# Kernel tuning notes

Measured on AMD Instinct MI355X. Metric: run time of the kernel, lower is better.

## Reference

```python
import jax, jax.numpy as jnp
import numpy as np

MAPP = jnp.array([0.5, 1.0, 1.5, 2.0], dtype=jnp.float32)  # magnitude constellation (len = one_hot_len)


def setup_inputs() -> dict:
    key = jax.random.key(0)
    ks = jax.random.split(key, 20)
    B, BL, SM = 512, 256, 8
    S = BL + SM            # sym_len = 264
    V, Z, OH = 128, 1024, 4
    inp = {}
    inp["l"] = 0
    inp["x_mag"] = jax.random.uniform(ks[0], (1, B, S), jnp.float32)
    inp["x_mag_oh"] = jax.random.normal(ks[1], (B, S * OH), jnp.float32)
    inp["v"] = jax.random.normal(ks[2], (B, V), jnp.float32)
    inp["x_phase"] = jax.random.normal(ks[3], (1, B, S), jnp.float32)
    inp["y_e"] = jax.random.normal(ks[4], (B, BL), jnp.float32)
    inp["y_o"] = jax.random.normal(ks[5], (B, BL), jnp.float32)
    inp["Psi_e"] = jax.random.normal(ks[6], (B, 2 * BL, 2 * S), jnp.float32) * 0.1
    inp["Psi_o"] = jax.random.normal(ks[7], (B, 2 * BL, 2 * S), jnp.float32) * 0.1
    # Linear params, std=0.01 as in torch init
    inp["W1"] = jax.random.normal(ks[8], (Z, S + V), jnp.float32) * 0.01
    inp["b1"] = jax.random.normal(ks[9], (Z,), jnp.float32) * 0.01
    inp["W2"] = jax.random.normal(ks[10], (S * OH, Z), jnp.float32) * 0.01
    inp["b2"] = jax.random.normal(ks[11], (S * OH,), jnp.float32) * 0.01
    inp["W3"] = jax.random.normal(ks[12], (V, Z), jnp.float32) * 0.01
    inp["b3"] = jax.random.normal(ks[13], (V,), jnp.float32) * 0.01
    inp["d1"] = jax.random.uniform(ks[14], (1,), jnp.float32)
    inp["d2"] = jax.random.uniform(ks[15], (1,), jnp.float32)
    inp["d3"] = jax.random.uniform(ks[16], (1,), jnp.float32)
    inp["d4"] = jax.random.uniform(ks[17], (1,), jnp.float32)
    return inp


def reference(l, x_mag, x_mag_oh, v, x_phase, y_e, y_o, Psi_e, Psi_o,
              W1, b1, W2, b2, W3, b3, d1, d2, d3, d4):
    B, S = x_phase.shape[1], x_phase.shape[2]
    BL = y_e.shape[1]
    mag, ph = x_mag[-1], x_phase[-1]          # [B,S]
    c, s = jnp.cos(ph), jnp.sin(ph)
    x = jnp.concatenate([mag * c, mag * s], axis=-1)  # [B,2S]

    def A_and_sql(Psi):
        # Psi: [B, 2*BL, 2*S]
        Px = jnp.einsum('bms,bs->bm', Psi, x)         # [B, 2*BL]
        a, b_ = Px[:, :BL], Px[:, BL:]
        # Psi^T @ blockdiag(a,b) == row-scale Psi (avoids diag_embed+bmm):
        # M[b,j,i] = Psi[b,j,i]*a[b,j] + Psi[b,BL+j,i]*b[b,j]  -> [B, BL, 2S]
        M = Psi[:, :BL, :] * a[:, :, None] + Psi[:, BL:, :] * b_[:, :, None]
        # jacobian @ (Psi^T D) == cos/sin row-scaling of the two S-halves:
        A = (c[:, :, None] * jnp.swapaxes(M[:, :, :S], 1, 2)
             + s[:, :, None] * jnp.swapaxes(M[:, :, S:], 1, 2))  # [B, S, BL]
        sql = a * a + b_ * b_                          # [B, BL]
        return A, sql

    A_e, sql_e = A_and_sql(Psi_e)
    A_o, sql_o = A_and_sql(Psi_o)
    mv = lambda A, y: jnp.einsum('bsk,bk->bs', A, y)
    # NOTE: original code uses delta2 for the A_o@y_o term (delta3 unused) -- kept faithful.
    q = (mag - d1 * mv(A_e, y_e) + d2 * mv(A_e, sql_e)
         - d2 * mv(A_o, y_o) + d4 * mv(A_o, sql_o))    # [B,S]

    z = jax.nn.relu(jnp.concatenate([q, v], axis=1) @ W1.T + b1)   # [B,Z]
    x_mag_oh_new = x_mag_oh + z @ W2.T + b2                        # [B,S*OH]
    # oh_2_sym: softmax over one-hot dim, expectation over constellation
    sym = jax.nn.softmax(x_mag_oh_new.reshape(B, S, -1), axis=-1) @ MAPP  # [B,S]
    x_mag_new = jnp.concatenate([x_mag, sym[None]], axis=0)
    v_new = v + z @ W3.T + b3
    return (x_mag_new, x_mag_oh_new, v_new)
```

## Files before the change

kernel.cpp:

```cpp
#include <hip/hip_runtime.h>

#define S_     264
#define BL_    256
#define TWO_S  528
#define TWO_BL 512
#define B_     512
#define V_     128
#define NQ     392
#define Z_     1024
#define N2_    1056
#define NTOT   1184

__global__ __launch_bounds__(256, 4) void k_psi(
    const float* __restrict__ x_mag, const float* __restrict__ x_phase,
    const float* __restrict__ y_e, const float* __restrict__ y_o,
    const float* __restrict__ Psi_e, const float* __restrict__ Psi_o,
    const float* __restrict__ d1, const float* __restrict__ d2,
    const float* __restrict__ d4,
    float* __restrict__ contrib)
{
    const int tid = threadIdx.x;
    const int b   = blockIdx.x >> 1;
    const int psi = blockIdx.x & 1;
    const float* Psi = psi ? Psi_o : Psi_e;
    const float* yv  = psi ? y_o  : y_e;
    const float coefY = psi ? -d2[0] : -d1[0];
    const float coefS = psi ?  d4[0] :  d2[0];

    __shared__ float4 xs4s[132];
    __shared__ float  cs[S_], sn[S_];
    __shared__ float  ys[BL_];
    __shared__ float4 redTy4[4][132];
    __shared__ float4 redTs4[4][132];

    float* xs = (float*)xs4s;

    for (int s = tid; s < S_; s += 256) {
        float mag = x_mag[(size_t)b * S_ + s];
        float ph  = x_phase[(size_t)b * S_ + s];
        float c = cosf(ph), si = sinf(ph);
        cs[s] = c; sn[s] = si;
        xs[s]      = mag * c;
        xs[S_ + s] = mag * si;
    }
    ys[tid] = yv[(size_t)b * BL_ + tid];
    __syncthreads();

    const int wave = tid >> 6, lane = tid & 63;
    const float4 f4z = {0.f, 0.f, 0.f, 0.f};

    float4 x0 = xs4s[lane];
    float4 x1 = xs4s[lane + 64];
    float4 x2 = (lane < 4) ? xs4s[lane + 128] : f4z;

    float4 ty0 = f4z, ty1 = f4z, ty2 = f4z;
    float4 ts0 = f4z, ts1 = f4z, ts2 = f4z;

    const float4* Pg = (const float4*)(Psi + (size_t)b * TWO_BL * TWO_S);

    int pair = wave;
    float4 l0, l1, l2 = f4z, h0, h1, h2 = f4z;
    {
        const float4* rl = Pg + (size_t)pair * 132;
        const float4* rh = rl + (size_t)BL_ * 132;
        l0 = rl[lane]; l1 = rl[lane + 64];
        h0 = rh[lane]; h1 = rh[lane + 64];
        if (lane < 4) { l2 = rl[lane + 128]; h2 = rh[lane + 128]; }
    }

    while (pair < BL_) {
        const int nxt = pair + 4;
        float4 nl0 = f4z, nl1 = f4z, nl2 = f4z;
        float4 nh0 = f4z, nh1 = f4z, nh2 = f4z;
        if (nxt < BL_) {
            const float4* rl = Pg + (size_t)nxt * 132;
            const float4* rh = rl + (size_t)BL_ * 132;
            nl0 = rl[lane]; nl1 = rl[lane + 64];
            nh0 = rh[lane]; nh1 = rh[lane + 64];
            if (lane < 4) { nl2 = rl[lane + 128]; nh2 = rh[lane + 128]; }
        }

        float a  = l0.x*x0.x + l0.y*x0.y + l0.z*x0.z + l0.w*x0.w
                 + l1.x*x1.x + l1.y*x1.y + l1.z*x1.z + l1.w*x1.w
                 + l2.x*x2.x + l2.y*x2.y + l2.z*x2.z + l2.w*x2.w;
        float bb = h0.x*x0.x + h0.y*x0.y + h0.z*x0.z + h0.w*x0.w
                 + h1.x*x1.x + h1.y*x1.y + h1.z*x1.z + h1.w*x1.w
                 + h2.x*x2.x + h2.y*x2.y + h2.z*x2.z + h2.w*x2.w;
        #pragma unroll
        for (int off = 32; off; off >>= 1) {
            a  += __shfl_xor(a, off);
            bb += __shfl_xor(bb, off);
        }

        const float yy  = ys[pair];
        const float sq  = a * a + bb * bb;
        const float cyl = a * yy, cyh = bb * yy;
        const float csl = a * sq, csh = bb * sq;

        ty0.x += l0.x*cyl + h0.x*cyh; ty0.y += l0.y*cyl + h0.y*cyh;
        ty0.z += l0.z*cyl + h0.z*cyh; ty0.w += l0.w*cyl + h0.w*cyh;
        ty1.x += l1.x*cyl + h1.x*cyh; ty1.y += l1.y*cyl + h1.y*cyh;
        ty1.z += l1.z*cyl + h1.z*cyh; ty1.w += l1.w*cyl + h1.w*cyh;
        ty2.x += l2.x*cyl + h2.x*cyh; ty2.y += l2.y*cyl + h2.y*cyh;
        ty2.z += l2.z*cyl + h2.z*cyh; ty2.w += l2.w*cyl + h2.w*cyh;

        ts0.x += l0.x*csl + h0.x*csh; ts0.y += l0.y*csl + h0.y*csh;
        ts0.z += l0.z*csl + h0.z*csh; ts0.w += l0.w*csl + h0.w*csh;
        ts1.x += l1.x*csl + h1.x*csh; ts1.y += l1.y*csl + h1.y*csh;
        ts1.z += l1.z*csl + h1.z*csh; ts1.w += l1.w*csl + h1.w*csh;
        ts2.x += l2.x*csl + h2.x*csh; ts2.y += l2.y*csl + h2.y*csh;
        ts2.z += l2.z*csl + h2.z*csh; ts2.w += l2.w*csl + h2.w*csh;

        pair = nxt;
        l0 = nl0; l1 = nl1; l2 = nl2;
        h0 = nh0; h1 = nh1; h2 = nh2;
    }

    redTy4[wave][lane]      = ty0;  redTy4[wave][lane + 64] = ty1;
    redTs4[wave][lane]      = ts0;  redTs4[wave][lane + 64] = ts1;
    if (lane < 4) {
        redTy4[wave][lane + 128] = ty2;
        redTs4[wave][lane + 128] = ts2;
    }
    __syncthreads();

    const float* redTy = (const float*)redTy4;
    const float* redTs = (const float*)redTs4;
    float* outp = contrib + (size_t)(b * 2 + psi) * S_;
    for (int s = tid; s < S_; s += 256) {
        float tyl = 0.f, tyh = 0.f, tsl = 0.f, tsh = 0.f;
        #pragma unroll
        for (int w = 0; w < 4; ++w) {
            tyl += redTy[w * TWO_S + s];
            tyh += redTy[w * TWO_S + S_ + s];
            tsl += redTs[w * TWO_S + s];
            tsh += redTs[w * TWO_S + S_ + s];
        }
        float mvy = cs[s] * tyl + sn[s] * tyh;
        float mvs = cs[s] * tsl + sn[s] * tsh;
        outp[s] = coefY * mvy + coefS * mvs;
    }
}

__global__ __launch_bounds__(256) void k_gemm1(
    const float* __restrict__ x_mag, const float* __restrict__ contrib,
    const float* __restrict__ v, const float* __restrict__ W1,
    const float* __restrict__ b1, float* __restrict__ z)
{
    const int tid = threadIdx.x;
    const int m0  = blockIdx.x * 32;
    const int n0  = blockIdx.y * 64;
    const int tr  = (tid >> 4) & 1 ? 0 : 0;
    const int trow = ((tid >> 4)) * 2;
    const int tcol = (tid & 15) * 4;

    __shared__ float As[16][36];
    __shared__ float Ws[16][68];

    float acc[2][4] = {};

    const int kr  = tid >> 2;
    const int kk4 = (tid & 3) * 4;

    for (int kc = 0; kc < NQ; kc += 16) {
        if (tid < 128) {
            const int arow = m0 + kr;
            const int gk = kc + kk4;
            float4 vv = {0.f, 0.f, 0.f, 0.f};
            if (gk < NQ) {
                if (gk + 3 < S_) {
                    float4 xm = *(const float4*)&x_mag[(size_t)arow * S_ + gk];
                    float4 ce = *(const float4*)&contrib[(size_t)(arow * 2) * S_ + gk];
                    float4 co = *(const float4*)&contrib[(size_t)(arow * 2 + 1) * S_ + gk];
                    vv.x = xm.x + ce.x + co.x; vv.y = xm.y + ce.y + co.y;
                    vv.z = xm.z + ce.z + co.z; vv.w = xm.w + ce.w + co.w;
                } else if (gk >= S_) {
                    vv = *(const float4*)&v[(size_t)arow * V_ + (gk - S_)];
                }
            }
            As[kk4 + 0][kr] = vv.x; As[kk4 + 1][kr] = vv.y;
            As[kk4 + 2][kr] = vv.z; As[kk4 + 3][kr] = vv.w;
        }
        {
            const int wrow = n0 + kr;
            const int gk = kc + kk4;
            float4 vv = {0.f, 0.f, 0.f, 0.f};
            if (gk + 3 < NQ) {
                vv = *(const float4*)&W1[(size_t)wrow * NQ + gk];
            } else if (gk < NQ) {
                const float* wp = W1 + (size_t)wrow * NQ + gk;
                vv.x = wp[0];
                if (gk + 1 < NQ) vv.y = wp[1];
                if (gk + 2 < NQ) vv.z = wp[2];
            }
            Ws[kk4 + 0][kr] = vv.x; Ws[kk4 + 1][kr] = vv.y;
            Ws[kk4 + 2][kr] = vv.z; Ws[kk4 + 3][kr] = vv.w;
        }
        __syncthreads();

        #pragma unroll
        for (int k = 0; k < 16; ++k) {
            float2 a2 = *(const float2*)&As[k][trow];
            float4 w4 = *(const float4*)&Ws[k][tcol];
            acc[0][0] += a2.x * w4.x; acc[0][1] += a2.x * w4.y;
            acc[0][2] += a2.x * w4.z; acc[0][3] += a2.x * w4.w;
            acc[1][0] += a2.y * w4.x; acc[1][1] += a2.y * w4.y;
            acc[1][2] += a2.y * w4.z; acc[1][3] += a2.y * w4.w;
        }
        __syncthreads();
    }

    #pragma unroll
    for (int i = 0; i < 2; ++i) {
        const int row = m0 + trow + i;
        const int col = n0 + tcol;
        float4 r;
        r.x = fmaxf(acc[i][0] + b1[col + 0], 0.f);
        r.y = fmaxf(acc[i][1] + b1[col + 1], 0.f);
        r.z = fmaxf(acc[i][2] + b1[col + 2], 0.f);
        r.w = fmaxf(acc[i][3] + b1[col + 3], 0.f);
        *(float4*)&z[(size_t)row * Z_ + col] = r;
    }
}

__global__ __launch_bounds__(256) void k_gemm23(
    const float* __restrict__ z,
    const float* __restrict__ W2, const float* __restrict__ b2,
    const float* __restrict__ oh,
    const float* __restrict__ W3, const float* __restrict__ b3,
    const float* __restrict__ v,
    float* __restrict__ out_oh, float* __restrict__ out_v)
{
    const int tid = threadIdx.x;
    const int m0  = blockIdx.x * 32;
    const int n0  = blockIdx.y * 64;
    const int trow = (tid >> 4) * 2;
    const int tcol = (tid & 15) * 4;

    __shared__ float As[16][36];
    __shared__ float Ws[16][68];

    float acc[2][4] = {};

    const int kr  = tid >> 2;
    const int kk4 = (tid & 3) * 4;

    for (int kc = 0; kc < Z_; kc += 16) {
        if (tid < 128) {
            const int arow = m0 + kr;
            float4 vv = *(const float4*)&z[(size_t)arow * Z_ + kc + kk4];
            As[kk4 + 0][kr] = vv.x; As[kk4 + 1][kr] = vv.y;
            As[kk4 + 2][kr] = vv.z; As[kk4 + 3][kr] = vv.w;
        }
        {
            const int wrow = n0 + kr;
            float4 vv = {0.f, 0.f, 0.f, 0.f};
            if (wrow < NTOT) {
                const float* wp = (wrow < N2_)
                    ? (W2 + (size_t)wrow * Z_)
                    : (W3 + (size_t)(wrow - N2_) * Z_);
                vv = *(const float4*)&wp[kc + kk4];
            }
            Ws[kk4 + 0][kr] = vv.x; Ws[kk4 + 1][kr] = vv.y;
            Ws[kk4 + 2][kr] = vv.z; Ws[kk4 + 3][kr] = vv.w;
        }
        __syncthreads();

        #pragma unroll
        for (int k = 0; k < 16; ++k) {
            float2 a2 = *(const float2*)&As[k][trow];
            float4 w4 = *(const float4*)&Ws[k][tcol];
            acc[0][0] += a2.x * w4.x; acc[0][1] += a2.x * w4.y;
            acc[0][2] += a2.x * w4.z; acc[0][3] += a2.x * w4.w;
            acc[1][0] += a2.y * w4.x; acc[1][1] += a2.y * w4.y;
            acc[1][2] += a2.y * w4.z; acc[1][3] += a2.y * w4.w;
        }
        __syncthreads();
    }

    #pragma unroll
    for (int i = 0; i < 2; ++i) {
        const int row = m0 + trow + i;
        const int col = n0 + tcol;
        if (col + 3 < N2_) {
            float4 ad = *(const float4*)&oh[(size_t)row * N2_ + col];
            float4 r;
            r.x = acc[i][0] + b2[col + 0] + ad.x;
            r.y = acc[i][1] + b2[col + 1] + ad.y;
            r.z = acc[i][2] + b2[col + 2] + ad.z;
            r.w = acc[i][3] + b2[col + 3] + ad.w;
            *(float4*)&out_oh[(size_t)row * N2_ + col] = r;
        } else if (col < NTOT) {
            const int c3 = col - N2_;
            float4 ad = *(const float4*)&v[(size_t)row * V_ + c3];
            float4 r;
            r.x = acc[i][0] + b3[c3 + 0] + ad.x;
            r.y = acc[i][1] + b3[c3 + 1] + ad.y;
            r.z = acc[i][2] + b3[c3 + 2] + ad.z;
            r.w = acc[i][3] + b3[c3 + 3] + ad.w;
            *(float4*)&out_v[(size_t)row * V_ + c3] = r;
        }
    }
}

__global__ void k_final(const float* __restrict__ x_mag,
                        const float* __restrict__ oh_new,
                        float* __restrict__ out0)
{
    int idx = blockIdx.x * 256 + threadIdx.x;
    if (idx >= B_ * S_) return;
    out0[idx] = x_mag[idx];
    const float* p = oh_new + (size_t)idx * 4;
    float a0 = p[0], a1 = p[1], a2 = p[2], a3 = p[3];
    float m  = fmaxf(fmaxf(a0, a1), fmaxf(a2, a3));
    float e0 = expf(a0 - m), e1 = expf(a1 - m), e2 = expf(a2 - m), e3 = expf(a3 - m);
    float sum = e0 + e1 + e2 + e3;
    float sym = (0.5f * e0 + 1.0f * e1 + 1.5f * e2 + 2.0f * e3) / sum;
    out0[B_ * S_ + idx] = sym;
}

extern "C" void kernel_launch(void* const* d_in, const int* in_sizes, int n_in,
                              void* d_out, int out_size, void* d_ws, size_t ws_size,
                              hipStream_t stream)
{
    const float* x_mag    = (const float*)d_in[1];
    const float* x_mag_oh = (const float*)d_in[2];
    const float* v        = (const float*)d_in[3];
    const float* x_phase  = (const float*)d_in[4];
    const float* y_e      = (const float*)d_in[5];
    const float* y_o      = (const float*)d_in[6];
    const float* Psi_e    = (const float*)d_in[7];
    const float* Psi_o    = (const float*)d_in[8];
    const float* W1       = (const float*)d_in[9];
    const float* b1       = (const float*)d_in[10];
    const float* W2       = (const float*)d_in[11];
    const float* b2       = (const float*)d_in[12];
    const float* W3       = (const float*)d_in[13];
    const float* b3       = (const float*)d_in[14];
    const float* d1       = (const float*)d_in[15];
    const float* d2       = (const float*)d_in[16];
    const float* d4       = (const float*)d_in[18];

    float* ws      = (float*)d_ws;
    float* contrib = ws;
    float* z       = contrib + 1024 * S_;

    float* out0   = (float*)d_out;
    float* out_oh = out0 + 2 * B_ * S_;
    float* out_v  = out_oh + B_ * N2_;

    k_psi<<<dim3(B_ * 2), dim3(256), 0, stream>>>(
        x_mag, x_phase, y_e, y_o, Psi_e, Psi_o, d1, d2, d4, contrib);

    k_gemm1<<<dim3(16, 16), dim3(256), 0, stream>>>(
        x_mag, contrib, v, W1, b1, z);

    k_gemm23<<<dim3(16, 19), dim3(256), 0, stream>>>(
        z, W2, b2, x_mag_oh, W3, b3, v, out_oh, out_v);

    k_final<<<dim3((B_ * S_ + 255) / 256), dim3(256), 0, stream>>>(
        x_mag, out_oh, out0);
}
```

Measured before the change: 314.1 us.

## Merge Psi accumulators, deepen prefetch, widen GEMM K tiles, fuse final softmax

The Psi kernel folds the y and squared-norm weights into a single scalar per row pair. That leaves one accumulator set instead of two, halving the FMA work and the shared reduction. It also double-buffers two row pairs ahead, so more global loads are in flight. Both GEMMs now stage 32-deep K tiles with all threads loading, which halves the barrier count. The separate final kernel is removed: the x_mag copy moves into the Psi kernel and the softmax expectation into the GEMM23 epilogue, saving a launch and a re-read of out_oh. The trade-off is higher register pressure in the Psi kernel and more shared memory in the GEMMs.

```diff
diff --git a/kernel.cpp b/kernel.cpp
--- a/kernel.cpp
+++ b/kernel.cpp
@@ -17,7 +17,7 @@
     const float* __restrict__ Psi_e, const float* __restrict__ Psi_o,
     const float* __restrict__ d1, const float* __restrict__ d2,
     const float* __restrict__ d4,
-    float* __restrict__ contrib)
+    float* __restrict__ contrib, float* __restrict__ out0)
 {
     const int tid = threadIdx.x;
     const int b   = blockIdx.x >> 1;
@@ -29,9 +29,8 @@
 
     __shared__ float4 xs4s[132];
     __shared__ float  cs[S_], sn[S_];
-    __shared__ float  ys[BL_];
-    __shared__ float4 redTy4[4][132];
-    __shared__ float4 redTs4[4][132];
+    __shared__ float  gys[BL_];
+    __shared__ float4 redU4[4][132];
 
     float* xs = (float*)xs4s;
 
@@ -42,8 +41,9 @@
         cs[s] = c; sn[s] = si;
         xs[s]      = mag * c;
         xs[S_ + s] = mag * si;
-    }
-    ys[tid] = yv[(size_t)b * BL_ + tid];
+        if (psi == 0) out0[(size_t)b * S_ + s] = mag;
+    }
+    gys[tid] = coefY * yv[(size_t)b * BL_ + tid];
     __syncthreads();
 
     const int wave = tid >> 6, lane = tid & 63;
@@ -53,92 +53,77 @@
     float4 x1 = xs4s[lane + 64];
     float4 x2 = (lane < 4) ? xs4s[lane + 128] : f4z;
 
-    float4 ty0 = f4z, ty1 = f4z, ty2 = f4z;
-    float4 ts0 = f4z, ts1 = f4z, ts2 = f4z;
+    float4 u0 = f4z, u1 = f4z, u2 = f4z;
 
     const float4* Pg = (const float4*)(Psi + (size_t)b * TWO_BL * TWO_S);
 
-    int pair = wave;
-    float4 l0, l1, l2 = f4z, h0, h1, h2 = f4z;
-    {
-        const float4* rl = Pg + (size_t)pair * 132;
-        const float4* rh = rl + (size_t)BL_ * 132;
-        l0 = rl[lane]; l1 = rl[lane + 64];
-        h0 = rh[lane]; h1 = rh[lane + 64];
-        if (lane < 4) { l2 = rl[lane + 128]; h2 = rh[lane + 128]; }
-    }
-
-    while (pair < BL_) {
-        const int nxt = pair + 4;
-        float4 nl0 = f4z, nl1 = f4z, nl2 = f4z;
-        float4 nh0 = f4z, nh1 = f4z, nh2 = f4z;
-        if (nxt < BL_) {
-            const float4* rl = Pg + (size_t)nxt * 132;
-            const float4* rh = rl + (size_t)BL_ * 132;
-            nl0 = rl[lane]; nl1 = rl[lane + 64];
-            nh0 = rh[lane]; nh1 = rh[lane + 64];
-            if (lane < 4) { nl2 = rl[lane + 128]; nh2 = rh[lane + 128]; }
-        }
-
-        float a  = l0.x*x0.x + l0.y*x0.y + l0.z*x0.z + l0.w*x0.w
-                 + l1.x*x1.x + l1.y*x1.y + l1.z*x1.z + l1.w*x1.w
-                 + l2.x*x2.x + l2.y*x2.y + l2.z*x2.z + l2.w*x2.w;
-        float bb = h0.x*x0.x + h0.y*x0.y + h0.z*x0.z + h0.w*x0.w
-                 + h1.x*x1.x + h1.y*x1.y + h1.z*x1.z + h1.w*x1.w
-                 + h2.x*x2.x + h2.y*x2.y + h2.z*x2.z + h2.w*x2.w;
-        #pragma unroll
-        for (int off = 32; off; off >>= 1) {
-            a  += __shfl_xor(a, off);
-            bb += __shfl_xor(bb, off);
-        }
-
-        const float yy  = ys[pair];
-        const float sq  = a * a + bb * bb;
-        const float cyl = a * yy, cyh = bb * yy;
-        const float csl = a * sq, csh = bb * sq;
-
-        ty0.x += l0.x*cyl + h0.x*cyh; ty0.y += l0.y*cyl + h0.y*cyh;
-        ty0.z += l0.z*cyl + h0.z*cyh; ty0.w += l0.w*cyl + h0.w*cyh;
-        ty1.x += l1.x*cyl + h1.x*cyh; ty1.y += l1.y*cyl + h1.y*cyh;
-        ty1.z += l1.z*cyl + h1.z*cyh; ty1.w += l1.w*cyl + h1.w*cyh;
-        ty2.x += l2.x*cyl + h2.x*cyh; ty2.y += l2.y*cyl + h2.y*cyh;
-        ty2.z += l2.z*cyl + h2.z*cyh; ty2.w += l2.w*cyl + h2.w*cyh;
-
-        ts0.x += l0.x*csl + h0.x*csh; ts0.y += l0.y*csl + h0.y*csh;
-        ts0.z += l0.z*csl + h0.z*csh; ts0.w += l0.w*csl + h0.w*csh;
-        ts1.x += l1.x*csl + h1.x*csh; ts1.y += l1.y*csl + h1.y*csh;
-        ts1.z += l1.z*csl + h1.z*csh; ts1.w += l1.w*csl + h1.w*csh;
-        ts2.x += l2.x*csl + h2.x*csh; ts2.y += l2.y*csl + h2.y*csh;
-        ts2.z += l2.z*csl + h2.z*csh; ts2.w += l2.w*csl + h2.w*csh;
-
-        pair = nxt;
-        l0 = nl0; l1 = nl1; l2 = nl2;
-        h0 = nh0; h1 = nh1; h2 = nh2;
-    }
-
-    redTy4[wave][lane]      = ty0;  redTy4[wave][lane + 64] = ty1;
-    redTs4[wave][lane]      = ts0;  redTs4[wave][lane + 64] = ts1;
-    if (lane < 4) {
-        redTy4[wave][lane + 128] = ty2;
-        redTs4[wave][lane + 128] = ts2;
-    }
+#define LOADF(PP, L0, L1, L2, H0, H1, H2) {                         \
+        const float4* rl_ = Pg + (size_t)(PP) * 132;                \
+        const float4* rh_ = rl_ + (size_t)BL_ * 132;                \
+        L0 = rl_[lane]; L1 = rl_[lane + 64];                        \
+        H0 = rh_[lane]; H1 = rh_[lane + 64];                        \
+        if (lane < 4) { L2 = rl_[lane + 128]; H2 = rh_[lane + 128]; } \
+        else          { L2 = f4z; H2 = f4z; }                       \
+    }
+
+#define COMPUTE(L0, L1, L2, H0, H1, H2, PIDX) {                     \
+        float a  = L0.x*x0.x + L0.y*x0.y + L0.z*x0.z + L0.w*x0.w    \
+                 + L1.x*x1.x + L1.y*x1.y + L1.z*x1.z + L1.w*x1.w    \
+                 + L2.x*x2.x + L2.y*x2.y + L2.z*x2.z + L2.w*x2.w;   \
+        float bb = H0.x*x0.x + H0.y*x0.y + H0.z*x0.z + H0.w*x0.w    \
+                 + H1.x*x1.x + H1.y*x1.y + H1.z*x1.z + H1.w*x1.w    \
+                 + H2.x*x2.x + H2.y*x2.y + H2.z*x2.z + H2.w*x2.w;   \
+        _Pragma("unroll")                                           \
+        for (int off_ = 32; off_; off_ >>= 1) {                     \
+            a  += __shfl_xor(a, off_);                              \
+            bb += __shfl_xor(bb, off_);                             \
+        }                                                           \
+        float g  = gys[PIDX] + coefS * (a * a + bb * bb);           \
+        float wl = a * g, wh = bb * g;                              \
+        u0.x += L0.x*wl + H0.x*wh;  u0.y += L0.y*wl + H0.y*wh;      \
+        u0.z += L0.z*wl + H0.z*wh;  u0.w += L0.w*wl + H0.w*wh;      \
+        u1.x += L1.x*wl + H1.x*wh;  u1.y += L1.y*wl + H1.y*wh;      \
+        u1.z += L1.z*wl + H1.z*wh;  u1.w += L1.w*wl + H1.w*wh;      \
+        u2.x += L2.x*wl + H2.x*wh;  u2.y += L2.y*wl + H2.y*wh;      \
+        u2.z += L2.z*wl + H2.z*wh;  u2.w += L2.w*wl + H2.w*wh;      \
+    }
+
+    float4 al0, al1, al2, ah0, ah1, ah2;
+    float4 bl0, bl1, bl2, bh0, bh1, bh2;
+    LOADF(wave,     al0, al1, al2, ah0, ah1, ah2);
+    LOADF(wave + 4, bl0, bl1, bl2, bh0, bh1, bh2);
+
+    for (int j = 0; j < 64; j += 2) {
+        const int pA = wave + 4 * j;
+        const int pC = (j + 2 < 64) ? pA + 8  : 0;
+        const int pD = (j + 3 < 64) ? pA + 12 : 0;
+        float4 cl0, cl1, cl2, ch0, ch1, ch2;
+        LOADF(pC, cl0, cl1, cl2, ch0, ch1, ch2);
+        COMPUTE(al0, al1, al2, ah0, ah1, ah2, pA);
+        float4 dl0, dl1, dl2, dh0, dh1, dh2;
+        LOADF(pD, dl0, dl1, dl2, dh0, dh1, dh2);
+        COMPUTE(bl0, bl1, bl2, bh0, bh1, bh2, pA + 4);
+        al0 = cl0; al1 = cl1; al2 = cl2; ah0 = ch0; ah1 = ch1; ah2 = ch2;
+        bl0 = dl0; bl1 = dl1; bl2 = dl2; bh0 = dh0; bh1 = dh1; bh2 = dh2;
+    }
+#undef LOADF
+#undef COMPUTE
+
+    redU4[wave][lane]      = u0;
+    redU4[wave][lane + 64] = u1;
+    if (lane < 4) redU4[wave][lane + 128] = u2;
     __syncthreads();
 
-    const float* redTy = (const float*)redTy4;
-    const float* redTs = (const float*)redTs4;
+    const float* redU = (const float*)redU4;
     float* outp = contrib + (size_t)(b * 2 + psi) * S_;
     for (int s = tid; s < S_; s += 256) {
-        float tyl = 0.f, tyh = 0.f, tsl = 0.f, tsh = 0.f;
+        float ul = 0.f, uh = 0.f;
         #pragma unroll
         for (int w = 0; w < 4; ++w) {
-            tyl += redTy[w * TWO_S + s];
-            tyh += redTy[w * TWO_S + S_ + s];
-            tsl += redTs[w * TWO_S + s];
-            tsh += redTs[w * TWO_S + S_ + s];
-        }
-        float mvy = cs[s] * tyl + sn[s] * tyh;
-        float mvs = cs[s] * tsl + sn[s] * tsh;
-        outp[s] = coefY * mvy + coefS * mvs;
+            ul += redU[w * TWO_S + s];
+            uh += redU[w * TWO_S + S_ + s];
+        }
+        outp[s] = cs[s] * ul + sn[s] * uh;
     }
 }
 
@@ -150,56 +135,48 @@
     const int tid = threadIdx.x;
     const int m0  = blockIdx.x * 32;
     const int n0  = blockIdx.y * 64;
-    const int tr  = (tid >> 4) & 1 ? 0 : 0;
-    const int trow = ((tid >> 4)) * 2;
+    const int trow = (tid >> 4) * 2;
     const int tcol = (tid & 15) * 4;
 
-    __shared__ float As[16][36];
-    __shared__ float Ws[16][68];
+    __shared__ float As[32][36];
+    __shared__ float Ws[32][68];
 
     float acc[2][4] = {};
 
-    const int kr  = tid >> 2;
-    const int kk4 = (tid & 3) * 4;
-
-    for (int kc = 0; kc < NQ; kc += 16) {
-        if (tid < 128) {
-            const int arow = m0 + kr;
-            const int gk = kc + kk4;
+    const int krA  = tid >> 3;
+    const int kkA  = (tid & 7) * 4;
+
+    for (int kc = 0; kc < NQ; kc += 32) {
+        {
+            const int arow = m0 + krA;
+            const int gk = kc + kkA;
             float4 vv = {0.f, 0.f, 0.f, 0.f};
-            if (gk < NQ) {
-                if (gk + 3 < S_) {
-                    float4 xm = *(const float4*)&x_mag[(size_t)arow * S_ + gk];
-                    float4 ce = *(const float4*)&contrib[(size_t)(arow * 2) * S_ + gk];
-                    float4 co = *(const float4*)&contrib[(size_t)(arow * 2 + 1) * S_ + gk];
-                    vv.x = xm.x + ce.x + co.x; vv.y = xm.y + ce.y + co.y;
-                    vv.z = xm.z + ce.z + co.z; vv.w = xm.w + ce.w + co.w;
-                } else if (gk >= S_) {
-                    vv = *(const float4*)&v[(size_t)arow * V_ + (gk - S_)];
-                }
+            if (gk < S_) {
+                float4 xm = *(const float4*)&x_mag[(size_t)arow * S_ + gk];
+                float4 ce = *(const float4*)&contrib[(size_t)(arow * 2) * S_ + gk];
+                float4 co = *(const float4*)&contrib[(size_t)(arow * 2 + 1) * S_ + gk];
+                vv.x = xm.x + ce.x + co.x; vv.y = xm.y + ce.y + co.y;
+                vv.z = xm.z + ce.z + co.z; vv.w = xm.w + ce.w + co.w;
+            } else if (gk < NQ) {
+                vv = *(const float4*)&v[(size_t)arow * V_ + (gk - S_)];
             }
-            As[kk4 + 0][kr] = vv.x; As[kk4 + 1][kr] = vv.y;
-            As[kk4 + 2][kr] = vv.z; As[kk4 + 3][kr] = vv.w;
-        }
-        {
-            const int wrow = n0 + kr;
-            const int gk = kc + kk4;
+            As[kkA + 0][krA] = vv.x; As[kkA + 1][krA] = vv.y;
+            As[kkA + 2][krA] = vv.z; As[kkA + 3][krA] = vv.w;
+        }
+        for (int i = tid; i < 512; i += 256) {
+            const int r  = i >> 3;
+            const int j4 = (i & 7) * 4;
+            const int gk = kc + j4;
             float4 vv = {0.f, 0.f, 0.f, 0.f};
-            if (gk + 3 < NQ) {
-                vv = *(const float4*)&W1[(size_t)wrow * NQ + gk];
-            } else if (gk < NQ) {
-                const float* wp = W1 + (size_t)wrow * NQ + gk;
-                vv.x = wp[0];
-                if (gk + 1 < NQ) vv.y = wp[1];
-                if (gk + 2 < NQ) vv.z = wp[2];
-            }
-            Ws[kk4 + 0][kr] = vv.x; Ws[kk4 + 1][kr] = vv.y;
-            Ws[kk4 + 2][kr] = vv.z; Ws[kk4 + 3][kr] = vv.w;
+            if (gk < NQ)
+                vv = *(const float4*)&W1[(size_t)(n0 + r) * NQ + gk];
+            Ws[j4 + 0][r] = vv.x; Ws[j4 + 1][r] = vv.y;
+            Ws[j4 + 2][r] = vv.z; Ws[j4 + 3][r] = vv.w;
         }
         __syncthreads();
 
         #pragma unroll
-        for (int k = 0; k < 16; ++k) {
+        for (int k = 0; k < 32; ++k) {
             float2 a2 = *(const float2*)&As[k][trow];
             float4 w4 = *(const float4*)&Ws[k][tcol];
             acc[0][0] += a2.x * w4.x; acc[0][1] += a2.x * w4.y;
@@ -229,7 +206,8 @@
     const float* __restrict__ oh,
     const float* __restrict__ W3, const float* __restrict__ b3,
     const float* __restrict__ v,
-    float* __restrict__ out_oh, float* __restrict__ out_v)
+    float* __restrict__ out_oh, float* __restrict__ out_v,
+    float* __restrict__ out0)
 {
     const int tid = threadIdx.x;
     const int m0  = blockIdx.x * 32;
@@ -237,37 +215,38 @@
     const int trow = (tid >> 4) * 2;
     const int tcol = (tid & 15) * 4;
 
-    __shared__ float As[16][36];
-    __shared__ float Ws[16][68];
+    __shared__ float As[32][36];
+    __shared__ float Ws[32][68];
 
     float acc[2][4] = {};
 
-    const int kr  = tid >> 2;
-    const int kk4 = (tid & 3) * 4;
-
-    for (int kc = 0; kc < Z_; kc += 16) {
-        if (tid < 128) {
-            const int arow = m0 + kr;
-            float4 vv = *(const float4*)&z[(size_t)arow * Z_ + kc + kk4];
-            As[kk4 + 0][kr] = vv.x; As[kk4 + 1][kr] = vv.y;
-            As[kk4 + 2][kr] = vv.z; As[kk4 + 3][kr] = vv.w;
-        }
+    const int krA = tid >> 3;
+    const int kkA = (tid & 7) * 4;
+
+    for (int kc = 0; kc < Z_; kc += 32) {
         {
-            const int wrow = n0 + kr;
+            float4 vv = *(const float4*)&z[(size_t)(m0 + krA) * Z_ + kc + kkA];
+            As[kkA + 0][krA] = vv.x; As[kkA + 1][krA] = vv.y;
+            As[kkA + 2][krA] = vv.z; As[kkA + 3][krA] = vv.w;
+        }
+        for (int i = tid; i < 512; i += 256) {
+            const int r  = i >> 3;
+            const int j4 = (i & 7) * 4;
+            const int wrow = n0 + r;
             float4 vv = {0.f, 0.f, 0.f, 0.f};
             if (wrow < NTOT) {
                 const float* wp = (wrow < N2_)
                     ? (W2 + (size_t)wrow * Z_)
                     : (W3 + (size_t)(wrow - N2_) * Z_);
-                vv = *(const float4*)&wp[kc + kk4];
+                vv = *(const float4*)&wp[kc + j4];
             }
-            Ws[kk4 + 0][kr] = vv.x; Ws[kk4 + 1][kr] = vv.y;
-            Ws[kk4 + 2][kr] = vv.z; Ws[kk4 + 3][kr] = vv.w;
+            Ws[j4 + 0][r] = vv.x; Ws[j4 + 1][r] = vv.y;
+            Ws[j4 + 2][r] = vv.z; Ws[j4 + 3][r] = vv.w;
         }
         __syncthreads();
 
         #pragma unroll
-        for (int k = 0; k < 16; ++k) {
+        for (int k = 0; k < 32; ++k) {
             float2 a2 = *(const float2*)&As[k][trow];
             float4 w4 = *(const float4*)&Ws[k][tcol];
             acc[0][0] += a2.x * w4.x; acc[0][1] += a2.x * w4.y;
@@ -282,7 +261,7 @@
     for (int i = 0; i < 2; ++i) {
         const int row = m0 + trow + i;
         const int col = n0 + tcol;
-        if (col + 3 < N2_) {
+        if (col < N2_) {
             float4 ad = *(const float4*)&oh[(size_t)row * N2_ + col];
             float4 r;
             r.x = acc[i][0] + b2[col + 0] + ad.x;
@@ -290,6 +269,12 @@
             r.z = acc[i][2] + b2[col + 2] + ad.z;
             r.w = acc[i][3] + b2[col + 3] + ad.w;
             *(float4*)&out_oh[(size_t)row * N2_ + col] = r;
+            float m  = fmaxf(fmaxf(r.x, r.y), fmaxf(r.z, r.w));
+            float e0 = expf(r.x - m), e1 = expf(r.y - m);
+            float e2 = expf(r.z - m), e3 = expf(r.w - m);
+            float sum = e0 + e1 + e2 + e3;
+            float sym = (0.5f * e0 + 1.0f * e1 + 1.5f * e2 + 2.0f * e3) / sum;
+            out0[(size_t)B_ * S_ + (size_t)row * S_ + (col >> 2)] = sym;
         } else if (col < NTOT) {
             const int c3 = col - N2_;
             float4 ad = *(const float4*)&v[(size_t)row * V_ + c3];
@@ -301,22 +286,6 @@
             *(float4*)&out_v[(size_t)row * V_ + c3] = r;
         }
     }
-}
-
-__global__ void k_final(const float* __restrict__ x_mag,
-                        const float* __restrict__ oh_new,
-                        float* __restrict__ out0)
-{
-    int idx = blockIdx.x * 256 + threadIdx.x;
-    if (idx >= B_ * S_) return;
-    out0[idx] = x_mag[idx];
-    const float* p = oh_new + (size_t)idx * 4;
-    float a0 = p[0], a1 = p[1], a2 = p[2], a3 = p[3];
-    float m  = fmaxf(fmaxf(a0, a1), fmaxf(a2, a3));
-    float e0 = expf(a0 - m), e1 = expf(a1 - m), e2 = expf(a2 - m), e3 = expf(a3 - m);
-    float sum = e0 + e1 + e2 + e3;
-    float sym = (0.5f * e0 + 1.0f * e1 + 1.5f * e2 + 2.0f * e3) / sum;
-    out0[B_ * S_ + idx] = sym;
 }
 
 extern "C" void kernel_launch(void* const* d_in, const int* in_sizes, int n_in,
@@ -350,14 +319,11 @@
     float* out_v  = out_oh + B_ * N2_;
 
     k_psi<<<dim3(B_ * 2), dim3(256), 0, stream>>>(
-        x_mag, x_phase, y_e, y_o, Psi_e, Psi_o, d1, d2, d4, contrib);
+        x_mag, x_phase, y_e, y_o, Psi_e, Psi_o, d1, d2, d4, contrib, out0);
 
     k_gemm1<<<dim3(16, 16), dim3(256), 0, stream>>>(
         x_mag, contrib, v, W1, b1, z);
 
     k_gemm23<<<dim3(16, 19), dim3(256), 0, stream>>>(
-        z, W2, b2, x_mag_oh, W3, b3, v, out_oh, out_v);
-
-    k_final<<<dim3((B_ * S_ + 255) / 256), dim3(256), 0, stream>>>(
-        x_mag, out_oh, out0);
+        z, W2, b2, x_mag_oh, W3, b3, v, out_oh, out_v, out0);
 }
```

After: 575.5 us. 83.2% more time.
